# Kernel optimization log

Hardware: AMD Instinct MI355X
Metric: run time of the kernel (lower is better)

The kernel has to match this reference:

```python
import jax, jax.numpy as jnp
import numpy as np

BITS = 8
SF = 4
KH, KW = 3, 3
PAD = 1
STRIDE = 1


def _linear_quantize(x, sf=SF, bits=BITS):
    # mirrors linear_quantize(..., return_type='float'):
    # x *= 2^(bits-1)/2^sf ; round (half-to-even, same as torch) ; clamp ; rescale back
    scale = 2.0 ** (bits - 1 - sf)
    bound = 2.0 ** (bits - 1)
    q = jnp.clip(jnp.round(x * scale), -bound, bound - 1.0)
    return q / scale


def _unfold(x, kh, kw, pad, stride):
    # torch.nn.functional.unfold ordering: features = (C, kh, kw)
    B, C, H, W = x.shape
    xp = jnp.pad(x, ((0, 0), (0, 0), (pad, pad), (pad, pad)))
    Ho = (H - kh + 2 * pad) // stride + 1
    Wo = (W - kw + 2 * pad) // stride + 1
    cols = []
    for i in range(kh):
        for j in range(kw):
            cols.append(xp[:, :, i:i + (Ho - 1) * stride + 1:stride,
                               j:j + (Wo - 1) * stride + 1:stride])
    p = jnp.stack(cols, axis=2)  # [B, C, kh*kw, Ho, Wo]
    return p.reshape(B, C * kh * kw, Ho * Wo), Ho, Wo


def setup_inputs() -> dict:
    key = jax.random.key(0)
    k1, k2, k3 = jax.random.split(key, 3)
    x = jax.random.normal(k1, (4, 64, 28, 28), dtype=jnp.float32)
    weight = jax.random.normal(k2, (64, 64, 3, 3), dtype=jnp.float32) * 0.05
    bias = jax.random.normal(k3, (64,), dtype=jnp.float32) * 0.05
    return {"x": x, "weight": weight, "bias": bias}


def reference(x, weight, bias):
    # conv2d_quant_forward with groups=1: quantize(x*w) elementwise,
    # quantize the summed accumulation, quantize after bias add.
    B = x.shape[0]
    O = weight.shape[0]
    inp_unf, Ho, Wo = _unfold(x, KH, KW, PAD, STRIDE)   # [B, CKK, L]
    w = weight.reshape(O, -1)                           # [O, CKK]
    # expanded elementwise product: [B, L, O, CKK]
    prod = inp_unf.transpose(0, 2, 1)[:, :, None, :] * w[None, None, :, :]
    prod = _linear_quantize(prod)
    out = _linear_quantize(prod.sum(axis=3))            # [B, L, O]
    out = _linear_quantize(out + bias[None, None, :])   # bias broadcast over L
    return out.transpose(0, 2, 1).reshape(B, O, Ho, Wo)
```

## Files before the change

### kernel.cpp

```cpp
#include <hip/hip_runtime.h>

static constexpr int C_IN  = 64;
static constexpr int O_OUT = 64;
static constexpr int HH    = 28;
static constexpr int WW    = 28;

__global__ __launch_bounds__(512, 8) void conv2d_quant_kernel(
    const float* __restrict__ x,
    const float* __restrict__ wgt,
    const float* __restrict__ bias,
    float* __restrict__ out)
{
    __shared__ float4 red4[8][64];

    const int tid = threadIdx.x;
    const int b   = blockIdx.z;
    const int y0  = blockIdx.y * 2;
    const int o0  = blockIdx.x * 4;

    const int lane = tid & 63;
    const int wid  = __builtin_amdgcn_readfirstlane(tid >> 6);
    const int l    = (lane < 56) ? lane : 0;
    const int row  = l / 28;
    const int px   = l - row * 28;

    int   off[9];
    float m8[9];
    #pragma unroll
    for (int i = 0; i < 3; ++i) {
        const int gy = y0 + row - 1 + i;
        const int cy = gy < 0 ? 0 : (gy > HH - 1 ? HH - 1 : gy);
        #pragma unroll
        for (int j = 0; j < 3; ++j) {
            const int gx = px - 1 + j;
            const int cx = gx < 0 ? 0 : (gx > WW - 1 ? WW - 1 : gx);
            const bool ok = ((unsigned)gy < (unsigned)HH) && ((unsigned)gx < (unsigned)WW);
            off[i * 3 + j] = cy * WW + cx;
            m8[i * 3 + j]  = ok ? 8.0f : 0.0f;
        }
    }

    const float* xp  = x + (b * C_IN + wid * 8) * (HH * WW);
    const float* wp0 = wgt + (o0 + 0) * (C_IN * 9) + wid * 8 * 9;
    const float* wp1 = wgt + (o0 + 1) * (C_IN * 9) + wid * 8 * 9;
    const float* wp2 = wgt + (o0 + 2) * (C_IN * 9) + wid * 8 * 9;
    const float* wp3 = wgt + (o0 + 3) * (C_IN * 9) + wid * 8 * 9;

    float a0 = 0.0f, a1 = 0.0f, a2 = 0.0f, a3 = 0.0f;

    #pragma unroll 2
    for (int c = 0; c < 8; ++c) {
        const float* xc = xp + c * (HH * WW);
        float xm[9];
        #pragma unroll
        for (int k = 0; k < 9; ++k)
            xm[k] = xc[off[k]] * m8[k];

        const float* wr0 = wp0 + c * 9;
        const float* wr1 = wp1 + c * 9;
        const float* wr2 = wp2 + c * 9;
        const float* wr3 = wp3 + c * 9;

        float s0 = 0.f, s1 = 0.f, s2 = 0.f, s3 = 0.f;
        #pragma unroll
        for (int k = 0; k < 9; ++k) {
            s0 += rintf(xm[k] * wr0[k]);
            s1 += rintf(xm[k] * wr1[k]);
            s2 += rintf(xm[k] * wr2[k]);
            s3 += rintf(xm[k] * wr3[k]);
        }
        a0 += s0; a1 += s1; a2 += s2; a3 += s3;
    }

    red4[wid][lane] = make_float4(a0, a1, a2, a3);
    __syncthreads();

    if (tid < 56) {
        float4 s = red4[0][tid];
        #pragma unroll
        for (int w = 1; w < 8; ++w) {
            const float4 p = red4[w][tid];
            s.x += p.x; s.y += p.y; s.z += p.z; s.w += p.w;
        }
        const float acc[4] = {s.x, s.y, s.z, s.w};
        const int row2 = tid / 28;
        const int px2  = tid - row2 * 28;
        const int y    = y0 + row2;
        #pragma unroll
        for (int q = 0; q < 4; ++q) {
            const float b8 = bias[o0 + q] * 8.0f;
            float v = fminf(fmaxf(acc[q], -128.0f), 127.0f);
            v = rintf(v + b8);
            v = fminf(fmaxf(v, -128.0f), 127.0f) * 0.125f;
            out[((b * O_OUT + o0 + q) * HH + y) * WW + px2] = v;
        }
    }
}

extern "C" void kernel_launch(void* const* d_in, const int* in_sizes, int n_in,
                              void* d_out, int out_size, void* d_ws, size_t ws_size,
                              hipStream_t stream)
{
    const float* x    = (const float*)d_in[0];
    const float* wgt  = (const float*)d_in[1];
    const float* bias = (const float*)d_in[2];
    float* out        = (float*)d_out;

    dim3 grid(16, 14, 4);
    conv2d_quant_kernel<<<grid, dim3(512), 0, stream>>>(x, wgt, bias, out);
}
```

Baseline: 18.98 us.

## Flatten pixel mapping so each wave covers 64 pixels across batch

Pixels are remapped so each block handles 64 consecutive flattened (batch, y, x) positions instead of two 28-pixel rows of one image. This uses all 64 lanes where 8 were idle before, and cuts the grid from 896 to 784 blocks. The channel loop is now fully unrolled, byte offsets are precomputed with the batch offset folded in, and the launch-bounds occupancy hint is lowered to 4, which may increase register use. Neighbouring pixels in a wave can now span image rows or batches, which makes gathers less regular.

```diff
diff --git a/kernel.cpp b/kernel.cpp
--- a/kernel.cpp
+++ b/kernel.cpp
@@ -4,8 +4,10 @@
 static constexpr int O_OUT = 64;
 static constexpr int HH    = 28;
 static constexpr int WW    = 28;
+static constexpr int CHW   = HH * WW;
+static constexpr int CKK   = C_IN * 9;
 
-__global__ __launch_bounds__(512, 8) void conv2d_quant_kernel(
+__global__ __launch_bounds__(512, 4) void conv2d_quant_kernel(
     const float* __restrict__ x,
     const float* __restrict__ wgt,
     const float* __restrict__ bias,
@@ -13,48 +15,51 @@
 {
     __shared__ float4 red4[8][64];
 
-    const int tid = threadIdx.x;
-    const int b   = blockIdx.z;
-    const int y0  = blockIdx.y * 2;
-    const int o0  = blockIdx.x * 4;
+    const int tid  = threadIdx.x;
+    const int pg   = blockIdx.y;
+    const int o0   = blockIdx.x * 4;
 
     const int lane = tid & 63;
     const int wid  = __builtin_amdgcn_readfirstlane(tid >> 6);
-    const int l    = (lane < 56) ? lane : 0;
-    const int row  = l / 28;
-    const int px   = l - row * 28;
 
-    int   off[9];
+    const int P   = pg * 64 + lane;
+    const int b   = P / CHW;
+    const int r   = P - b * CHW;
+    const int y   = r / WW;
+    const int xc0 = r - y * WW;
+
+    int   offB[9];
     float m8[9];
     #pragma unroll
     for (int i = 0; i < 3; ++i) {
-        const int gy = y0 + row - 1 + i;
+        const int gy = y - 1 + i;
         const int cy = gy < 0 ? 0 : (gy > HH - 1 ? HH - 1 : gy);
         #pragma unroll
         for (int j = 0; j < 3; ++j) {
-            const int gx = px - 1 + j;
+            const int gx = xc0 - 1 + j;
             const int cx = gx < 0 ? 0 : (gx > WW - 1 ? WW - 1 : gx);
             const bool ok = ((unsigned)gy < (unsigned)HH) && ((unsigned)gx < (unsigned)WW);
-            off[i * 3 + j] = cy * WW + cx;
-            m8[i * 3 + j]  = ok ? 8.0f : 0.0f;
+            offB[i * 3 + j] = (b * (C_IN * CHW) + cy * WW + cx) * 4;
+            m8[i * 3 + j]   = ok ? 8.0f : 0.0f;
         }
     }
 
-    const float* xp  = x + (b * C_IN + wid * 8) * (HH * WW);
-    const float* wp0 = wgt + (o0 + 0) * (C_IN * 9) + wid * 8 * 9;
-    const float* wp1 = wgt + (o0 + 1) * (C_IN * 9) + wid * 8 * 9;
-    const float* wp2 = wgt + (o0 + 2) * (C_IN * 9) + wid * 8 * 9;
-    const float* wp3 = wgt + (o0 + 3) * (C_IN * 9) + wid * 8 * 9;
+    const char* xw = (const char*)(x + (wid * 8) * CHW);
+
+    const float* wp0 = wgt + (o0 + 0) * CKK + wid * 72;
+    const float* wp1 = wgt + (o0 + 1) * CKK + wid * 72;
+    const float* wp2 = wgt + (o0 + 2) * CKK + wid * 72;
+    const float* wp3 = wgt + (o0 + 3) * CKK + wid * 72;
 
     float a0 = 0.0f, a1 = 0.0f, a2 = 0.0f, a3 = 0.0f;
 
-    #pragma unroll 2
+    #pragma unroll
     for (int c = 0; c < 8; ++c) {
-        const float* xc = xp + c * (HH * WW);
+        const char* xcb = xw + c * (CHW * 4);
         float xm[9];
         #pragma unroll
         for (int k = 0; k < 9; ++k)
-            xm[k] = xc[off[k]] * m8[k];
+            xm[k] = *(const float*)(xcb + offB[k]) * m8[k];
 
         const float* wr0 = wp0 + c * 9;
         const float* wr1 = wp1 + c * 9;
@@ -75,24 +80,24 @@
     red4[wid][lane] = make_float4(a0, a1, a2, a3);
     __syncthreads();
 
-    if (tid < 56) {
+    if (tid < 64) {
         float4 s = red4[0][tid];
         #pragma unroll
         for (int w = 1; w < 8; ++w) {
             const float4 p = red4[w][tid];
             s.x += p.x; s.y += p.y; s.z += p.z; s.w += p.w;
         }
+        const int P2  = pg * 64 + tid;
+        const int b2  = P2 / CHW;
+        const int r2  = P2 - b2 * CHW;
         const float acc[4] = {s.x, s.y, s.z, s.w};
-        const int row2 = tid / 28;
-        const int px2  = tid - row2 * 28;
-        const int y    = y0 + row2;
         #pragma unroll
         for (int q = 0; q < 4; ++q) {
             const float b8 = bias[o0 + q] * 8.0f;
             float v = fminf(fmaxf(acc[q], -128.0f), 127.0f);
             v = rintf(v + b8);
             v = fminf(fmaxf(v, -128.0f), 127.0f) * 0.125f;
-            out[((b * O_OUT + o0 + q) * HH + y) * WW + px2] = v;
+            out[(b2 * O_OUT + o0 + q) * CHW + r2] = v;
         }
     }
 }
@@ -106,6 +111,6 @@
     const float* bias = (const float*)d_in[2];
     float* out        = (float*)d_out;
 
-    dim3 grid(16, 14, 4);
+    dim3 grid(16, 49, 1);
     conv2d_quant_kernel<<<grid, dim3(512), 0, stream>>>(x, wgt, bias, out);
 }
```

New measurement: 20.95 us. 10.4% more time.
